# Kernel optimization log

Measured on AMD Instinct MI355X. Metric: run time of the kernel, lower is better.

## Reference

```python
import jax, jax.numpy as jnp
import numpy as np

THRESH = 0.9   # config['thresh_cnn']
R = 2          # config['radius'] -> maxpool kernel 2R+1=5, stride 1, padding R


def setup_inputs() -> dict:
    key = jax.random.key(0)
    # [B=1, C=1, D=64, H=512, W=512]
    pred_vol = jax.random.uniform(key, (1, 1, 64, 512, 512), dtype=jnp.float32)
    return {"pred_vol": pred_vol}


def reference(pred_vol):
    # threshold: keep values > thresh, else 0
    pred_thresh = jnp.where(pred_vol > THRESH, pred_vol, 0.0)
    # 3D max-pool, kernel 2R+1, stride 1, padding R (torch pads with -inf for maxpool)
    k = 2 * R + 1
    mp = jax.lax.reduce_window(
        pred_thresh, -jnp.inf, jax.lax.max,
        window_dimensions=(1, 1, k, k, k),
        window_strides=(1, 1, 1, 1, 1),
        padding=[(0, 0), (0, 0), (R, R), (R, R), (R, R)],
    )
    # keep only strict local maxima of the thresholded volume
    conf_vol = jnp.where((mp > 0.0) & (mp == pred_thresh), mp, 0.0)
    return jnp.squeeze(conf_vol)  # [D, H, W] dense peak confidence map
```

## Files before the change

### kernel.cpp

```cpp
#include <hip/hip_runtime.h>


#define THRESH 0.9f

constexpr int D = 64, H = 512, W = 512;
constexpr int TW = 64;
constexpr int TH = 16;
constexpr int DCHUNK = 8;
constexpr int HALO = 2;
constexpr int LROWS = TH + 2 * HALO;
constexpr int RAWQ  = TW / 4 + 2;
constexpr int RAWQ_S = RAWQ + 1;
constexpr int WMQ   = TW / 4;
constexpr int WMQ_S = WMQ + 1;
constexpr int NS = DCHUNK + 2 * HALO;

typedef float floatx4 __attribute__((ext_vector_type(4)));

__device__ __forceinline__ void barrier_no_drain() {
    asm volatile("s_waitcnt lgkmcnt(0)\n\ts_barrier" ::: "memory");
}

__device__ __forceinline__ float4 thresh4(float4 v) {
    v.x = (v.x > THRESH) ? v.x : 0.f;
    v.y = (v.y > THRESH) ? v.y : 0.f;
    v.z = (v.z > THRESH) ? v.z : 0.f;
    v.w = (v.w > THRESH) ? v.w : 0.f;
    return v;
}

__device__ __forceinline__ float4 max4(float4 a, float4 b) {
    return make_float4(fmaxf(a.x, b.x), fmaxf(a.y, b.y),
                       fmaxf(a.z, b.z), fmaxf(a.w, b.w));
}

__device__ __forceinline__ float4 wmax5(float4 a, float4 b, float4 c) {
    const float f2 = a.z, f3 = a.w, f4 = b.x, f5 = b.y, f6 = b.z, f7 = b.w;
    const float f8 = c.x, f9 = c.y;
    const float m45 = fmaxf(f4, f5);
    const float m56 = fmaxf(f5, f6);
    const float m345 = fmaxf(f3, m45);
    const float m456 = fmaxf(f4, m56);
    const float m567 = fmaxf(m56, f7);
    const float m678 = fmaxf(fmaxf(f6, f7), f8);
    float4 r;
    r.x = fmaxf(fmaxf(f2, f6), m345);
    r.y = fmaxf(fmaxf(f3, f7), m456);
    r.z = fmaxf(fmaxf(f4, f8), m567);
    r.w = fmaxf(fmaxf(f5, f9), m678);
    return r;
}

__global__ __launch_bounds__(256)
void peak3d_kernel(const float* __restrict__ in, float* __restrict__ out) {
    __shared__ float4 raw[LROWS * RAWQ_S];
    __shared__ float4 wm [LROWS * WMQ_S];

    const int tx = threadIdx.x;
    const int ty = threadIdx.y;
    const int tid = ty * 16 + tx;

    const int w0 = blockIdx.x * TW;
    const int h0 = blockIdx.y * TH;
    const int d0 = blockIdx.z * DCHUNK;

    const int q0 = tid;
    const int q1 = tid + 256;
    const int r0 = q0 / RAWQ, c0 = q0 % RAWQ;
    const int r1 = q1 / RAWQ, c1 = q1 % RAWQ;
    const int lds0 = r0 * RAWQ_S + c0;
    const int lds1 = r1 * RAWQ_S + c1;
    const int gh0 = h0 + r0 - HALO, gw0 = w0 + 4 * c0 - 4;
    const int gh1 = h0 + r1 - HALO, gw1 = w0 + 4 * c1 - 4;
    const bool has1 = (q1 < LROWS * RAWQ);
    const bool ib0 = (gh0 >= 0 && gh0 < H && gw0 >= 0 && gw0 < W);
    const bool ib1 = has1 && (gh1 >= 0 && gh1 < H && gw1 >= 0 && gw1 < W);
    const size_t off0 = ib0 ? ((size_t)gh0 * W + gw0) : 0;
    const size_t off1 = ib1 ? ((size_t)gh1 * W + gw1) : 0;

    const float4 zero4 = make_float4(0.f, 0.f, 0.f, 0.f);
    float4 win[5], cen[5];
#pragma unroll
    for (int k = 0; k < 5; ++k) { win[k] = zero4; cen[k] = zero4; }

    auto loadSlice = [&](int dd, float4& a, float4& b) {
        a = zero4; b = zero4;
        if (dd >= 0 && dd < D) {
            const size_t base = (size_t)dd * (H * W);
            if (ib0) a = thresh4(*reinterpret_cast<const float4*>(in + base + off0));
            if (ib1) b = thresh4(*reinterpret_cast<const float4*>(in + base + off1));
        }
    };

    float4 pfa[2], pfb[2];
    loadSlice(d0 - HALO + 0, pfa[0], pfb[0]);
    loadSlice(d0 - HALO + 1, pfa[1], pfb[1]);

#pragma unroll
    for (int t = 0; t < NS; ++t) {
        const int slot = t & 1;

        raw[lds0] = pfa[slot];
        if (has1) raw[lds1] = pfb[slot];
        if (t + 2 < NS) loadSlice(d0 - HALO + t + 2, pfa[slot], pfb[slot]);

        barrier_no_drain();

        {
            const float4* rp = &raw[ty * RAWQ_S + tx];
            wm[ty * WMQ_S + tx] = wmax5(rp[0], rp[1], rp[2]);
            if (tid < (LROWS - TH) * WMQ) {
                const int r = TH + (tid >> 4), c = tid & 15;
                const float4* rq = &raw[r * RAWQ_S + c];
                wm[r * WMQ_S + c] = wmax5(rq[0], rq[1], rq[2]);
            }
            cen[t % 5] = raw[(ty + HALO) * RAWQ_S + (tx + 1)];
        }

        barrier_no_drain();

        {
            const float4* wp = &wm[ty * WMQ_S + tx];
            float4 hv = wp[0];
            hv = max4(hv, wp[1 * WMQ_S]);
            hv = max4(hv, wp[2 * WMQ_S]);
            hv = max4(hv, wp[3 * WMQ_S]);
            hv = max4(hv, wp[4 * WMQ_S]);
            win[t % 5] = hv;

            if (t >= 4) {
                const int dout = d0 + (t - 4);
                const float4 mp = max4(max4(max4(win[0], win[1]),
                                            max4(win[2], win[3])), win[4]);
                const float4 tcc = cen[(t + 3) % 5];
                floatx4 res;
                res.x = (mp.x > 0.f && mp.x == tcc.x) ? mp.x : 0.f;
                res.y = (mp.y > 0.f && mp.y == tcc.y) ? mp.y : 0.f;
                res.z = (mp.z > 0.f && mp.z == tcc.z) ? mp.z : 0.f;
                res.w = (mp.w > 0.f && mp.w == tcc.w) ? mp.w : 0.f;
                floatx4* op = reinterpret_cast<floatx4*>(
                    out + (size_t)dout * (H * W) +
                    (size_t)(h0 + ty) * W + (w0 + 4 * tx));
                __builtin_nontemporal_store(res, op);
            }
        }
    }
}

extern "C" void kernel_launch(void* const* d_in, const int* in_sizes, int n_in,
                              void* d_out, int out_size, void* d_ws, size_t ws_size,
                              hipStream_t stream) {
    const float* in = (const float*)d_in[0];
    float* out = (float*)d_out;
    dim3 grid(W / TW, H / TH, D / DCHUNK);
    dim3 block(16, 16, 1);
    hipLaunchKernelGGL(peak3d_kernel, grid, block, 0, stream, in, out);
}
```

Before: 125.9 us.

## Restructure 3D peak kernel: vertical-first max, shuffle horizontal pass, deeper depth chunks

Removes the intermediate LDS stage for the horizontal max. Each thread now takes a 5-row vertical max from double-buffered LDS, then does the 5-wide horizontal max with wavefront shuffles plus edge-column reads. This drops one barrier per depth slice. The per-load threshold is removed and applied only in the final peak test (c > THRESH and mp == c). That is equivalent to the original because a kept centre above the threshold is unaffected by smaller sub-threshold neighbours. DCHUNK doubles to 16, cutting redundant depth-halo loads per output, but the grid has fewer blocks and each thread carries more serial work.

```diff
diff --git a/kernel.cpp b/kernel.cpp
--- a/kernel.cpp
+++ b/kernel.cpp
@@ -4,15 +4,14 @@
 #define THRESH 0.9f
 
 constexpr int D = 64, H = 512, W = 512;
+constexpr int HW = H * W;
 constexpr int TW = 64;
 constexpr int TH = 16;
-constexpr int DCHUNK = 8;
+constexpr int DCHUNK = 16;
 constexpr int HALO = 2;
 constexpr int LROWS = TH + 2 * HALO;
 constexpr int RAWQ  = TW / 4 + 2;
-constexpr int RAWQ_S = RAWQ + 1;
-constexpr int WMQ   = TW / 4;
-constexpr int WMQ_S = WMQ + 1;
+constexpr int RAW_S = RAWQ + 1;
 constexpr int NS = DCHUNK + 2 * HALO;
 
 typedef float floatx4 __attribute__((ext_vector_type(4)));
@@ -21,22 +20,14 @@
     asm volatile("s_waitcnt lgkmcnt(0)\n\ts_barrier" ::: "memory");
 }
 
-__device__ __forceinline__ float4 thresh4(float4 v) {
-    v.x = (v.x > THRESH) ? v.x : 0.f;
-    v.y = (v.y > THRESH) ? v.y : 0.f;
-    v.z = (v.z > THRESH) ? v.z : 0.f;
-    v.w = (v.w > THRESH) ? v.w : 0.f;
-    return v;
-}
-
 __device__ __forceinline__ float4 max4(float4 a, float4 b) {
     return make_float4(fmaxf(a.x, b.x), fmaxf(a.y, b.y),
                        fmaxf(a.z, b.z), fmaxf(a.w, b.w));
 }
 
-__device__ __forceinline__ float4 wmax5(float4 a, float4 b, float4 c) {
-    const float f2 = a.z, f3 = a.w, f4 = b.x, f5 = b.y, f6 = b.z, f7 = b.w;
-    const float f8 = c.x, f9 = c.y;
+__device__ __forceinline__ float4 wmax5s(float f2, float f3, float4 b,
+                                         float f8, float f9) {
+    const float f4 = b.x, f5 = b.y, f6 = b.z, f7 = b.w;
     const float m45 = fmaxf(f4, f5);
     const float m56 = fmaxf(f5, f6);
     const float m345 = fmaxf(f3, m45);
@@ -53,8 +44,7 @@
 
 __global__ __launch_bounds__(256)
 void peak3d_kernel(const float* __restrict__ in, float* __restrict__ out) {
-    __shared__ float4 raw[LROWS * RAWQ_S];
-    __shared__ float4 wm [LROWS * WMQ_S];
+    __shared__ float4 raw[2][LROWS * RAW_S];
 
     const int tx = threadIdx.x;
     const int ty = threadIdx.y;
@@ -68,8 +58,8 @@
     const int q1 = tid + 256;
     const int r0 = q0 / RAWQ, c0 = q0 % RAWQ;
     const int r1 = q1 / RAWQ, c1 = q1 % RAWQ;
-    const int lds0 = r0 * RAWQ_S + c0;
-    const int lds1 = r1 * RAWQ_S + c1;
+    const int lds0 = r0 * RAW_S + c0;
+    const int lds1 = r1 * RAW_S + c1;
     const int gh0 = h0 + r0 - HALO, gw0 = w0 + 4 * c0 - 4;
     const int gh1 = h0 + r1 - HALO, gw1 = w0 + 4 * c1 - 4;
     const bool has1 = (q1 < LROWS * RAWQ);
@@ -86,9 +76,9 @@
     auto loadSlice = [&](int dd, float4& a, float4& b) {
         a = zero4; b = zero4;
         if (dd >= 0 && dd < D) {
-            const size_t base = (size_t)dd * (H * W);
-            if (ib0) a = thresh4(*reinterpret_cast<const float4*>(in + base + off0));
-            if (ib1) b = thresh4(*reinterpret_cast<const float4*>(in + base + off1));
+            const size_t base = (size_t)dd * HW;
+            if (ib0) a = *reinterpret_cast<const float4*>(in + base + off0);
+            if (ib1) b = *reinterpret_cast<const float4*>(in + base + off1);
         }
     };
 
@@ -96,53 +86,56 @@
     loadSlice(d0 - HALO + 0, pfa[0], pfb[0]);
     loadSlice(d0 - HALO + 1, pfa[1], pfb[1]);
 
+    const int hcol = (tx == 0) ? 0 : (RAWQ - 1);
+
 #pragma unroll
     for (int t = 0; t < NS; ++t) {
-        const int slot = t & 1;
+        const int buf = t & 1;
 
-        raw[lds0] = pfa[slot];
-        if (has1) raw[lds1] = pfb[slot];
-        if (t + 2 < NS) loadSlice(d0 - HALO + t + 2, pfa[slot], pfb[slot]);
+        raw[buf][lds0] = pfa[buf];
+        if (has1) raw[buf][lds1] = pfb[buf];
+        if (t + 2 < NS) loadSlice(d0 - HALO + t + 2, pfa[buf], pfb[buf]);
 
         barrier_no_drain();
 
-        {
-            const float4* rp = &raw[ty * RAWQ_S + tx];
-            wm[ty * WMQ_S + tx] = wmax5(rp[0], rp[1], rp[2]);
-            if (tid < (LROWS - TH) * WMQ) {
-                const int r = TH + (tid >> 4), c = tid & 15;
-                const float4* rq = &raw[r * RAWQ_S + c];
-                wm[r * WMQ_S + c] = wmax5(rq[0], rq[1], rq[2]);
-            }
-            cen[t % 5] = raw[(ty + HALO) * RAWQ_S + (tx + 1)];
-        }
+        const float4* bp = &raw[buf][0];
+        const float4 r0q = bp[(ty + 0) * RAW_S + (tx + 1)];
+        const float4 r1q = bp[(ty + 1) * RAW_S + (tx + 1)];
+        const float4 r2q = bp[(ty + 2) * RAW_S + (tx + 1)];
+        const float4 r3q = bp[(ty + 3) * RAW_S + (tx + 1)];
+        const float4 r4q = bp[(ty + 4) * RAW_S + (tx + 1)];
+        const float4 hv = max4(max4(max4(r0q, r1q), max4(r3q, r4q)), r2q);
 
-        barrier_no_drain();
+        const float4 e0 = bp[(ty + 0) * RAW_S + hcol];
+        const float4 e1 = bp[(ty + 1) * RAW_S + hcol];
+        const float4 e2 = bp[(ty + 2) * RAW_S + hcol];
+        const float4 e3 = bp[(ty + 3) * RAW_S + hcol];
+        const float4 e4 = bp[(ty + 4) * RAW_S + hcol];
+        const float4 hq = max4(max4(max4(e0, e1), max4(e3, e4)), e2);
 
-        {
-            const float4* wp = &wm[ty * WMQ_S + tx];
-            float4 hv = wp[0];
-            hv = max4(hv, wp[1 * WMQ_S]);
-            hv = max4(hv, wp[2 * WMQ_S]);
-            hv = max4(hv, wp[3 * WMQ_S]);
-            hv = max4(hv, wp[4 * WMQ_S]);
-            win[t % 5] = hv;
+        float f2 = __shfl_up(hv.z, 1);
+        float f3 = __shfl_up(hv.w, 1);
+        float f8 = __shfl_down(hv.x, 1);
+        float f9 = __shfl_down(hv.y, 1);
+        if (tx == 0)  { f2 = hq.z; f3 = hq.w; }
+        if (tx == 15) { f8 = hq.x; f9 = hq.y; }
 
-            if (t >= 4) {
-                const int dout = d0 + (t - 4);
-                const float4 mp = max4(max4(max4(win[0], win[1]),
-                                            max4(win[2], win[3])), win[4]);
-                const float4 tcc = cen[(t + 3) % 5];
-                floatx4 res;
-                res.x = (mp.x > 0.f && mp.x == tcc.x) ? mp.x : 0.f;
-                res.y = (mp.y > 0.f && mp.y == tcc.y) ? mp.y : 0.f;
-                res.z = (mp.z > 0.f && mp.z == tcc.z) ? mp.z : 0.f;
-                res.w = (mp.w > 0.f && mp.w == tcc.w) ? mp.w : 0.f;
-                floatx4* op = reinterpret_cast<floatx4*>(
-                    out + (size_t)dout * (H * W) +
-                    (size_t)(h0 + ty) * W + (w0 + 4 * tx));
-                __builtin_nontemporal_store(res, op);
-            }
+        win[t % 5] = wmax5s(f2, f3, hv, f8, f9);
+        cen[t % 5] = r2q;
+
+        if (t >= 4) {
+            const int dout = d0 + (t - 4);
+            const float4 mp = max4(max4(max4(win[0], win[1]),
+                                        max4(win[2], win[3])), win[4]);
+            const float4 c = cen[(t + 3) % 5];
+            floatx4 res;
+            res.x = (c.x > THRESH && mp.x == c.x) ? c.x : 0.f;
+            res.y = (c.y > THRESH && mp.y == c.y) ? c.y : 0.f;
+            res.z = (c.z > THRESH && mp.z == c.z) ? c.z : 0.f;
+            res.w = (c.w > THRESH && mp.w == c.w) ? c.w : 0.f;
+            floatx4* op = reinterpret_cast<floatx4*>(
+                out + (size_t)dout * HW + (size_t)(h0 + ty) * W + (w0 + 4 * tx));
+            __builtin_nontemporal_store(res, op);
         }
     }
 }
```

Result: faster. 116.6 us (-7.3%).
